# Optimization experiments

Measured on AMD Instinct MI355X. Metric: run time of the kernel, lower is better.

Reference implementation:

```python
import jax, jax.numpy as jnp
import numpy as np

B, N, H_IN, H_HID, N_HEAD = 32, 500, 64, 16, 8
N_VALID = 400  # valid (non-padded) nodes per graph; node 0 is the root
NEG_INF = -1e20


def setup_inputs() -> dict:
    key = jax.random.key(0)
    ks = jax.random.split(key, 10)
    x = jax.random.normal(ks[0], (B, N, H_IN), jnp.float32)
    # sparse-ish binary adjacency with self loops
    A = (jax.random.uniform(ks[1], (B, N, N)) < 0.05).astype(jnp.float32)
    A = jnp.maximum(A, jnp.eye(N, dtype=jnp.float32)[None])
    # mask_nonzero: first N_VALID nodes of every graph are valid
    mask_batch = jnp.repeat(jnp.arange(B, dtype=jnp.int32), N_VALID)
    mask_row = jnp.tile(jnp.arange(N_VALID, dtype=jnp.int32), B)
    s = 0.1
    w1 = jax.random.normal(ks[2], (N_HEAD, H_IN, H_HID), jnp.float32) * s
    a_src1 = jax.random.normal(ks[3], (N_HEAD, H_HID), jnp.float32) * s
    a_dst1 = jax.random.normal(ks[4], (N_HEAD, H_HID), jnp.float32) * s
    w2 = jax.random.normal(ks[5], (1, N_HEAD * H_HID, H_IN), jnp.float32) * s
    a_src2 = jax.random.normal(ks[6], (1, H_IN), jnp.float32) * s
    a_dst2 = jax.random.normal(ks[7], (1, H_IN), jnp.float32) * s
    attn_w = jax.random.normal(ks[8], (2 * H_IN,), jnp.float32) * s
    return {"x": x, "A": A, "mask_batch": mask_batch, "mask_row": mask_row,
            "w1": w1, "a_src1": a_src1, "a_dst1": a_dst1,
            "w2": w2, "a_src2": a_src2, "a_dst2": a_dst2, "attn_w": attn_w}


def gat_layer(h_in, A, w, a_src, a_dst):
    # h_in: [B,N,F_in]; w: [H,F_in,F_out]
    h = jnp.einsum('bnf,hfo->bhno', h_in, w)              # [B,H,N,F_out]
    e_src = jnp.einsum('bhno,ho->bhn', h, a_src)          # [B,H,N]
    e_dst = jnp.einsum('bhno,ho->bhn', h, a_dst)
    e = jax.nn.leaky_relu(e_src[..., :, None] + e_dst[..., None, :], 0.2)  # [B,H,N,N]
    e = jnp.where(A[:, None, :, :] > 0, e, NEG_INF)
    attn = jax.nn.softmax(e, axis=-1)
    return jnp.einsum('bhnm,bhmo->bhno', attn, h)         # [B,H,N,F_out]


def reference(x, A, mask_batch, mask_row, w1, a_src1, a_dst1, w2, a_src2, a_dst2, attn_w):
    b, n, _ = x.shape
    # BatchGAT encoder: layer 1 (multi-head, concat + ELU), layer 2 (1 head -> h_in)
    h1 = gat_layer(x, A, w1, a_src1, a_dst1)                       # [B,H,N,h_hid]
    h1 = jax.nn.elu(h1).transpose(0, 2, 1, 3).reshape(b, n, -1)    # [B,N,H*h_hid]
    xc = gat_layer(h1, A, w2, a_src2, a_dst2)[:, 0]                # [B,N,h_in]
    # zero out padded nodes (so their Post_Attn scores are exactly 0)
    valid = jnp.zeros((b, n), x.dtype).at[mask_batch, mask_row].set(1.0)
    xc = xc * valid[:, :, None]
    # Post_Attn: scatter root features to each valid node position
    root = jnp.zeros_like(xc).at[mask_batch, mask_row, :].set(xc[mask_batch, 0, :])
    x_plus = jnp.concatenate([xc, root], axis=-1)                  # [B,N,2*h_in]
    score = x_plus @ attn_w                                        # [B,N]
    score = jnp.where(score == 0, NEG_INF, score)[:, :, None]      # masked_fill
    attn = jax.nn.softmax(score, axis=1)                           # softmax over nodes
    pooled = jnp.einsum('bnf,bn->bf', xc, attn[:, :, 0])           # [B,h_in]
    return pooled, attn
```

## Files before the change

### kernel.cpp

```cpp
#include <hip/hip_runtime.h>

#define NB 32
#define NN 500
#define HIN 64
#define HHID 16
#define NHEAD 8
#define NVALID 400
#define MAXK 128
#define NEG_INF -1e20f

__global__ __launch_bounds__(256) void k_pre(const float* __restrict__ A,
                                             int* __restrict__ nbr, int* __restrict__ cnt,
                                             const float* __restrict__ x, const float* __restrict__ w1,
                                             const float* __restrict__ as1, const float* __restrict__ ad1,
                                             float* __restrict__ h1p, float* __restrict__ e1s,
                                             float* __restrict__ e1d)
{
    int bid = blockIdx.x;
    if (bid < 4000) {
        int row = bid * 4 + (threadIdx.x >> 6);
        int lane = threadIdx.x & 63;
        const float4* arow4 = (const float4*)(A + (size_t)row * NN);
        int* np = nbr + (size_t)row * MAXK;
        int c = 0;
#pragma unroll
        for (int it = 0; it < 2; ++it) {
            int idx = it * 64 + lane;
            float4 av;
            if (idx < 125) av = arow4[idx];
            else { av.x = av.y = av.z = av.w = 0.f; }
            bool v0 = av.x > 0.f, v1 = av.y > 0.f, v2 = av.z > 0.f, v3 = av.w > 0.f;
            unsigned long long b0 = __ballot(v0), b1 = __ballot(v1);
            unsigned long long b2 = __ballot(v2), b3 = __ballot(v3);
            unsigned long long below = (1ull << lane) - 1ull;
            int p = c + __popcll(b0 & below) + __popcll(b1 & below)
                      + __popcll(b2 & below) + __popcll(b3 & below);
            int col = idx * 4;
            if (v0 && p < MAXK) np[p] = col;     p += (int)v0;
            if (v1 && p < MAXK) np[p] = col + 1; p += (int)v1;
            if (v2 && p < MAXK) np[p] = col + 2; p += (int)v2;
            if (v3 && p < MAXK) np[p] = col + 3; p += (int)v3;
            c += (int)(__popcll(b0) + __popcll(b1) + __popcll(b2) + __popcll(b3));
        }
        if (lane == 0) cnt[row] = c < MAXK ? c : MAXK;
        return;
    }
    int pb = bid - 4000;
    int b = pb >> 5, chunk = pb & 31;
    int t = threadIdx.x, slot = t >> 7, lane = t & 127;
    int h = lane >> 4, o = lane & 15;
    float wreg[64];
#pragma unroll
    for (int f = 0; f < 64; ++f) wreg[f] = w1[h * 1024 + f * 16 + o];
    float as_r = as1[h * 16 + o], ad_r = ad1[h * 16 + o];
    __shared__ __align__(16) float xs[2][64];
    for (int i = 0; i < 8; ++i) {
        int n = chunk * 16 + i * 2 + slot;
        bool valid = n < NN;
        if (valid && lane < 64) xs[slot][lane] = x[(size_t)(b * NN + n) * HIN + lane];
        __syncthreads();
        if (valid) {
            float acc = 0.f;
#pragma unroll
            for (int f4 = 0; f4 < 16; ++f4) {
                float4 xv = *(const float4*)&xs[slot][f4 * 4];
                acc += xv.x * wreg[f4 * 4] + xv.y * wreg[f4 * 4 + 1]
                     + xv.z * wreg[f4 * 4 + 2] + xv.w * wreg[f4 * 4 + 3];
            }
            h1p[(size_t)(b * NN + n) * 128 + lane] = acc;
            float vs = acc * as_r, vd = acc * ad_r;
#pragma unroll
            for (int m = 1; m < 16; m <<= 1) { vs += __shfl_xor(vs, m); vd += __shfl_xor(vd, m); }
            if (o == 0) {
                e1s[(size_t)(b * NN + n) * 8 + h] = vs;
                e1d[(size_t)(b * NN + n) * 8 + h] = vd;
            }
        }
        __syncthreads();
    }
}

__global__ __launch_bounds__(128) void k_agg1(const int* __restrict__ nbr, const int* __restrict__ cnt,
                                              const float* __restrict__ h1p, const float* __restrict__ e1s,
                                              const float* __restrict__ e1d, float* __restrict__ h1cat)
{
    int row = blockIdx.x;
    int b = row / NN, n = row - b * NN;
    (void)n;
    int t = threadIdx.x;
    int h = t >> 4, o = t & 15;
    __shared__ int nb_s[MAXK];
    __shared__ float p_s[NHEAD][MAXK];
    int K = cnt[row];
    for (int k = t; k < K; k += 128) nb_s[k] = nbr[(size_t)row * MAXK + k];
    __syncthreads();
    float es = e1s[(size_t)row * 8 + h];
    float r[8];
    float mx = -1e30f;
#pragma unroll
    for (int j = 0; j < 8; ++j) {
        int k = o + j * 16;
        if (k < K) {
            float e = es + e1d[(size_t)(b * NN + nb_s[k]) * 8 + h];
            e = e > 0.f ? e : 0.2f * e;
            r[j] = e;
            mx = fmaxf(mx, e);
        }
    }
#pragma unroll
    for (int m = 1; m < 16; m <<= 1) mx = fmaxf(mx, __shfl_xor(mx, m));
    float sum = 0.f;
#pragma unroll
    for (int j = 0; j < 8; ++j) {
        int k = o + j * 16;
        if (k < K) { float v = __expf(r[j] - mx); r[j] = v; sum += v; }
    }
#pragma unroll
    for (int m = 1; m < 16; m <<= 1) sum += __shfl_xor(sum, m);
    float inv = 1.f / sum;
#pragma unroll
    for (int j = 0; j < 8; ++j) {
        int k = o + j * 16;
        if (k < K) p_s[h][k] = r[j] * inv;
    }
    __syncthreads();
    float acc = 0.f;
    const float* hp = h1p + (size_t)b * NN * 128 + t;
    for (int k = 0; k < K; ++k) acc += p_s[h][k] * hp[(size_t)nb_s[k] * 128];
    float outv = acc > 0.f ? acc : expm1f(acc);
    h1cat[(size_t)row * 128 + t] = outv;
}

__global__ __launch_bounds__(256) void k_proj2(const float* __restrict__ h1cat, const float* __restrict__ w2,
                                               const float* __restrict__ as2, const float* __restrict__ ad2,
                                               float* __restrict__ h2p, float* __restrict__ e2s,
                                               float* __restrict__ e2d)
{
    int b = blockIdx.y, chunk = blockIdx.x;
    int t = threadIdx.x, slot = t >> 7, lane = t & 127;
    int fh = lane >> 6, o = lane & 63;
    float wreg[64];
#pragma unroll
    for (int j = 0; j < 64; ++j) wreg[j] = w2[(fh * 64 + j) * 64 + o];
    float as_r = as2[o], ad_r = ad2[o];
    __shared__ __align__(16) float xs[2][128];
    __shared__ float part[2][128];
    for (int i = 0; i < 8; ++i) {
        int n = chunk * 16 + i * 2 + slot;
        bool valid = n < NN;
        if (valid) xs[slot][lane] = h1cat[(size_t)(b * NN + n) * 128 + lane];
        __syncthreads();
        float acc = 0.f;
        if (valid) {
#pragma unroll
            for (int j4 = 0; j4 < 16; ++j4) {
                float4 xv = *(const float4*)&xs[slot][fh * 64 + j4 * 4];
                acc += xv.x * wreg[j4 * 4] + xv.y * wreg[j4 * 4 + 1]
                     + xv.z * wreg[j4 * 4 + 2] + xv.w * wreg[j4 * 4 + 3];
            }
        }
        part[slot][lane] = acc;
        __syncthreads();
        if (valid && fh == 0) {
            float val = acc + part[slot][64 + o];
            h2p[(size_t)(b * NN + n) * 64 + o] = val;
            float vs = val * as_r, vd = val * ad_r;
#pragma unroll
            for (int m = 1; m < 64; m <<= 1) { vs += __shfl_xor(vs, m); vd += __shfl_xor(vd, m); }
            if (o == 0) { e2s[b * NN + n] = vs; e2d[b * NN + n] = vd; }
        }
        __syncthreads();
    }
}

__global__ __launch_bounds__(64) void k_agg2(const int* __restrict__ nbr, const int* __restrict__ cnt,
                                             const float* __restrict__ h2p, const float* __restrict__ e2s,
                                             const float* __restrict__ e2d, const float* __restrict__ aw,
                                             float* __restrict__ xc, float* __restrict__ sc,
                                             float* __restrict__ root_dot)
{
    int row = blockIdx.x;
    int b = row / NN, n = row - b * NN;
    int t = threadIdx.x;
    if (n >= NVALID) { xc[(size_t)row * 64 + t] = 0.f; return; }
    __shared__ int nb_s[MAXK];
    __shared__ float p_s[MAXK];
    int K = cnt[row];
    for (int k = t; k < K; k += 64) nb_s[k] = nbr[(size_t)row * MAXK + k];
    __syncthreads();
    float es = e2s[row];
    float r0 = -1e30f, r1 = -1e30f;
    if (t < K) {
        float e = es + e2d[b * NN + nb_s[t]];
        r0 = e > 0.f ? e : 0.2f * e;
    }
    if (t + 64 < K) {
        float e = es + e2d[b * NN + nb_s[t + 64]];
        r1 = e > 0.f ? e : 0.2f * e;
    }
    float mx = fmaxf(r0, r1);
#pragma unroll
    for (int m = 1; m < 64; m <<= 1) mx = fmaxf(mx, __shfl_xor(mx, m));
    float v0 = (t < K) ? __expf(r0 - mx) : 0.f;
    float v1 = (t + 64 < K) ? __expf(r1 - mx) : 0.f;
    float sum = v0 + v1;
#pragma unroll
    for (int m = 1; m < 64; m <<= 1) sum += __shfl_xor(sum, m);
    float inv = 1.f / sum;
    if (t < K) p_s[t] = v0 * inv;
    if (t + 64 < K) p_s[t + 64] = v1 * inv;
    __syncthreads();
    float acc = 0.f;
    for (int k = 0; k < K; ++k) acc += p_s[k] * h2p[(size_t)(b * NN + nb_s[k]) * 64 + t];
    xc[(size_t)row * 64 + t] = acc;
    float v = acc * aw[t];
#pragma unroll
    for (int m = 1; m < 64; m <<= 1) v += __shfl_xor(v, m);
    if (t == 0) sc[row] = v;
    if (n == 0) {
        float v2 = acc * aw[64 + t];
#pragma unroll
        for (int m = 1; m < 64; m <<= 1) v2 += __shfl_xor(v2, m);
        if (t == 0) root_dot[b] = v2;
    }
}

__global__ __launch_bounds__(1024) void k_pool(const float* __restrict__ xc, const float* __restrict__ sc,
                                               const float* __restrict__ root_dot, float* __restrict__ out)
{
    int b = blockIdx.x;
    int t = threadIdx.x, w = t >> 6, lane = t & 63;
    __shared__ float attn_s[NN];
    __shared__ float red[16];
    __shared__ float part[16][64];
    const float* xb = xc + (size_t)b * NN * 64;
    float rd = root_dot[b];
    float s = NEG_INF;
    if (t < NVALID) {
        s = sc[b * NN + t] + rd;
        if (s == 0.f) s = NEG_INF;
    }
    float mx = s;
#pragma unroll
    for (int m = 1; m < 64; m <<= 1) mx = fmaxf(mx, __shfl_xor(mx, m));
    if (lane == 0) red[w] = mx;
    __syncthreads();
    mx = red[0];
#pragma unroll
    for (int i = 1; i < 16; ++i) mx = fmaxf(mx, red[i]);
    float e = (t < NN) ? __expf(s - mx) : 0.f;
    float sum = e;
#pragma unroll
    for (int m = 1; m < 64; m <<= 1) sum += __shfl_xor(sum, m);
    __syncthreads();
    if (lane == 0) red[w] = sum;
    __syncthreads();
    sum = 0.f;
#pragma unroll
    for (int i = 0; i < 16; ++i) sum += red[i];
    float inv = 1.f / sum;
    if (t < NN) {
        float a = e * inv;
        out[NB * 64 + b * NN + t] = a;
        attn_s[t] = a;
    }
    __syncthreads();
    float acc = 0.f;
    for (int n = w; n < NN; n += 16) acc += attn_s[n] * xb[(size_t)n * 64 + lane];
    part[w][lane] = acc;
    __syncthreads();
    if (t < 64) {
        float v = 0.f;
#pragma unroll
        for (int i = 0; i < 16; ++i) v += part[i][t];
        out[b * 64 + t] = v;
    }
}

extern "C" void kernel_launch(void* const* d_in, const int* in_sizes, int n_in,
                              void* d_out, int out_size, void* d_ws, size_t ws_size,
                              hipStream_t stream) {
    const float* x   = (const float*)d_in[0];
    const float* A   = (const float*)d_in[1];
    const float* w1  = (const float*)d_in[4];
    const float* as1 = (const float*)d_in[5];
    const float* ad1 = (const float*)d_in[6];
    const float* w2  = (const float*)d_in[7];
    const float* as2 = (const float*)d_in[8];
    const float* ad2 = (const float*)d_in[9];
    const float* aw  = (const float*)d_in[10];
    float* out = (float*)d_out;

    char* ws = (char*)d_ws;
    int* nbr = (int*)ws;
    int* cnt = (int*)(ws + (size_t)16000 * 128 * 4);
    float* f = (float*)(ws + (size_t)16000 * 129 * 4);
    float* h1p   = f;  f += (size_t)NB * NN * 128;
    float* e1s   = f;  f += (size_t)NB * NN * NHEAD;
    float* e1d   = f;  f += (size_t)NB * NN * NHEAD;
    float* h1cat = f;  f += (size_t)NB * NN * 128;
    float* h2p   = f;  f += (size_t)NB * NN * 64;
    float* e2s   = f;  f += (size_t)NB * NN;
    float* e2d   = f;  f += (size_t)NB * NN;
    float* xc    = f;  f += (size_t)NB * NN * 64;
    float* sc    = f;  f += (size_t)NB * NN;
    float* rootd = f;  f += NB;

    hipLaunchKernelGGL(k_pre,   dim3(5024),   dim3(256), 0, stream, A, nbr, cnt, x, w1, as1, ad1, h1p, e1s, e1d);
    hipLaunchKernelGGL(k_agg1,  dim3(NB * NN), dim3(128), 0, stream, nbr, cnt, h1p, e1s, e1d, h1cat);
    hipLaunchKernelGGL(k_proj2, dim3(32, NB), dim3(256), 0, stream, h1cat, w2, as2, ad2, h2p, e2s, e2d);
    hipLaunchKernelGGL(k_agg2,  dim3(NB * NN), dim3(64), 0, stream, nbr, cnt, h2p, e2s, e2d, aw, xc, sc, rootd);
    hipLaunchKernelGGL(k_pool,  dim3(NB),     dim3(1024), 0, stream, xc, sc, rootd, out);
}
```

Measured before the change: 169.5 us.

## Fuse layer-2 projection into aggregation and pooling into last-block epilogue

Folds the layer-2 projection (h1cat @ w2 plus attention logits) into the layer-1 aggregation kernel, so the h1cat intermediate is no longer written to and read back from global memory. The final pooling kernel is merged into the layer-2 aggregation using a per-graph atomic counter, and the last block to finish each graph does the softmax and weighted sum. This takes five launches down to three. In exchange, every aggregation block now loads 64 weights per thread, and the pooling tail runs on a single 64-thread block per graph, which serialises the 500-node reduction.

```diff
diff --git a/kernel.cpp b/kernel.cpp
--- a/kernel.cpp
+++ b/kernel.cpp
@@ -14,9 +14,10 @@
                                              const float* __restrict__ x, const float* __restrict__ w1,
                                              const float* __restrict__ as1, const float* __restrict__ ad1,
                                              float* __restrict__ h1p, float* __restrict__ e1s,
-                                             float* __restrict__ e1d)
+                                             float* __restrict__ e1d, int* __restrict__ poolcnt)
 {
     int bid = blockIdx.x;
+    if (bid == 0 && threadIdx.x < NB) poolcnt[threadIdx.x] = 0;
     if (bid < 4000) {
         int row = bid * 4 + (threadIdx.x >> 6);
         int lane = threadIdx.x & 63;
@@ -80,17 +81,26 @@
     }
 }
 
-__global__ __launch_bounds__(128) void k_agg1(const int* __restrict__ nbr, const int* __restrict__ cnt,
-                                              const float* __restrict__ h1p, const float* __restrict__ e1s,
-                                              const float* __restrict__ e1d, float* __restrict__ h1cat)
+__global__ __launch_bounds__(128) void k_mid(const int* __restrict__ nbr, const int* __restrict__ cnt,
+                                             const float* __restrict__ h1p, const float* __restrict__ e1s,
+                                             const float* __restrict__ e1d, const float* __restrict__ w2,
+                                             const float* __restrict__ as2, const float* __restrict__ ad2,
+                                             float* __restrict__ h2p, float* __restrict__ e2s,
+                                             float* __restrict__ e2d)
 {
     int row = blockIdx.x;
-    int b = row / NN, n = row - b * NN;
-    (void)n;
+    int b = row / NN;
     int t = threadIdx.x;
     int h = t >> 4, o = t & 15;
+    int half = t >> 6, o2 = t & 63;
+    float wreg[64];
+    const float* wp = w2 + (size_t)(half * 64) * 64 + o2;
+#pragma unroll
+    for (int j = 0; j < 64; ++j) wreg[j] = wp[j * 64];
     __shared__ int nb_s[MAXK];
     __shared__ float p_s[NHEAD][MAXK];
+    __shared__ float hc[128];
+    __shared__ float part[128];
     int K = cnt[row];
     for (int k = t; k < K; k += 128) nb_s[k] = nbr[(size_t)row * MAXK + k];
     __syncthreads();
@@ -127,154 +137,134 @@
     float acc = 0.f;
     const float* hp = h1p + (size_t)b * NN * 128 + t;
     for (int k = 0; k < K; ++k) acc += p_s[h][k] * hp[(size_t)nb_s[k] * 128];
-    float outv = acc > 0.f ? acc : expm1f(acc);
-    h1cat[(size_t)row * 128 + t] = outv;
+    hc[t] = acc > 0.f ? acc : expm1f(acc);
+    __syncthreads();
+    float acc2 = 0.f;
+#pragma unroll
+    for (int j = 0; j < 64; ++j) acc2 += hc[half * 64 + j] * wreg[j];
+    part[t] = acc2;
+    __syncthreads();
+    if (half == 0) {
+        float val = acc2 + part[64 + o2];
+        h2p[(size_t)row * 64 + o2] = val;
+        float vs = val * as2[o2], vd = val * ad2[o2];
+#pragma unroll
+        for (int m = 1; m < 64; m <<= 1) { vs += __shfl_xor(vs, m); vd += __shfl_xor(vd, m); }
+        if (o2 == 0) { e2s[row] = vs; e2d[row] = vd; }
+    }
 }
 
-__global__ __launch_bounds__(256) void k_proj2(const float* __restrict__ h1cat, const float* __restrict__ w2,
-                                               const float* __restrict__ as2, const float* __restrict__ ad2,
-                                               float* __restrict__ h2p, float* __restrict__ e2s,
-                                               float* __restrict__ e2d)
-{
-    int b = blockIdx.y, chunk = blockIdx.x;
-    int t = threadIdx.x, slot = t >> 7, lane = t & 127;
-    int fh = lane >> 6, o = lane & 63;
-    float wreg[64];
-#pragma unroll
-    for (int j = 0; j < 64; ++j) wreg[j] = w2[(fh * 64 + j) * 64 + o];
-    float as_r = as2[o], ad_r = ad2[o];
-    __shared__ __align__(16) float xs[2][128];
-    __shared__ float part[2][128];
-    for (int i = 0; i < 8; ++i) {
-        int n = chunk * 16 + i * 2 + slot;
-        bool valid = n < NN;
-        if (valid) xs[slot][lane] = h1cat[(size_t)(b * NN + n) * 128 + lane];
-        __syncthreads();
-        float acc = 0.f;
-        if (valid) {
-#pragma unroll
-            for (int j4 = 0; j4 < 16; ++j4) {
-                float4 xv = *(const float4*)&xs[slot][fh * 64 + j4 * 4];
-                acc += xv.x * wreg[j4 * 4] + xv.y * wreg[j4 * 4 + 1]
-                     + xv.z * wreg[j4 * 4 + 2] + xv.w * wreg[j4 * 4 + 3];
-            }
-        }
-        part[slot][lane] = acc;
-        __syncthreads();
-        if (valid && fh == 0) {
-            float val = acc + part[slot][64 + o];
-            h2p[(size_t)(b * NN + n) * 64 + o] = val;
-            float vs = val * as_r, vd = val * ad_r;
-#pragma unroll
-            for (int m = 1; m < 64; m <<= 1) { vs += __shfl_xor(vs, m); vd += __shfl_xor(vd, m); }
-            if (o == 0) { e2s[b * NN + n] = vs; e2d[b * NN + n] = vd; }
-        }
-        __syncthreads();
-    }
-}
-
-__global__ __launch_bounds__(64) void k_agg2(const int* __restrict__ nbr, const int* __restrict__ cnt,
+__global__ __launch_bounds__(64) void k_last(const int* __restrict__ nbr, const int* __restrict__ cnt,
                                              const float* __restrict__ h2p, const float* __restrict__ e2s,
                                              const float* __restrict__ e2d, const float* __restrict__ aw,
                                              float* __restrict__ xc, float* __restrict__ sc,
-                                             float* __restrict__ root_dot)
+                                             float* __restrict__ root_dot, int* __restrict__ poolcnt,
+                                             float* __restrict__ out)
 {
     int row = blockIdx.x;
     int b = row / NN, n = row - b * NN;
     int t = threadIdx.x;
-    if (n >= NVALID) { xc[(size_t)row * 64 + t] = 0.f; return; }
     __shared__ int nb_s[MAXK];
     __shared__ float p_s[MAXK];
-    int K = cnt[row];
-    for (int k = t; k < K; k += 64) nb_s[k] = nbr[(size_t)row * MAXK + k];
-    __syncthreads();
-    float es = e2s[row];
-    float r0 = -1e30f, r1 = -1e30f;
-    if (t < K) {
-        float e = es + e2d[b * NN + nb_s[t]];
-        r0 = e > 0.f ? e : 0.2f * e;
-    }
-    if (t + 64 < K) {
-        float e = es + e2d[b * NN + nb_s[t + 64]];
-        r1 = e > 0.f ? e : 0.2f * e;
-    }
-    float mx = fmaxf(r0, r1);
-#pragma unroll
-    for (int m = 1; m < 64; m <<= 1) mx = fmaxf(mx, __shfl_xor(mx, m));
-    float v0 = (t < K) ? __expf(r0 - mx) : 0.f;
-    float v1 = (t + 64 < K) ? __expf(r1 - mx) : 0.f;
-    float sum = v0 + v1;
-#pragma unroll
-    for (int m = 1; m < 64; m <<= 1) sum += __shfl_xor(sum, m);
-    float inv = 1.f / sum;
-    if (t < K) p_s[t] = v0 * inv;
-    if (t + 64 < K) p_s[t + 64] = v1 * inv;
-    __syncthreads();
-    float acc = 0.f;
-    for (int k = 0; k < K; ++k) acc += p_s[k] * h2p[(size_t)(b * NN + nb_s[k]) * 64 + t];
-    xc[(size_t)row * 64 + t] = acc;
-    float v = acc * aw[t];
-#pragma unroll
-    for (int m = 1; m < 64; m <<= 1) v += __shfl_xor(v, m);
-    if (t == 0) sc[row] = v;
-    if (n == 0) {
-        float v2 = acc * aw[64 + t];
-#pragma unroll
-        for (int m = 1; m < 64; m <<= 1) v2 += __shfl_xor(v2, m);
-        if (t == 0) root_dot[b] = v2;
-    }
-}
-
-__global__ __launch_bounds__(1024) void k_pool(const float* __restrict__ xc, const float* __restrict__ sc,
-                                               const float* __restrict__ root_dot, float* __restrict__ out)
-{
-    int b = blockIdx.x;
-    int t = threadIdx.x, w = t >> 6, lane = t & 63;
     __shared__ float attn_s[NN];
-    __shared__ float red[16];
-    __shared__ float part[16][64];
+    __shared__ int isLast;
+    if (n >= NVALID) {
+        xc[(size_t)row * 64 + t] = 0.f;
+    } else {
+        int K = cnt[row];
+        for (int k = t; k < K; k += 64) nb_s[k] = nbr[(size_t)row * MAXK + k];
+        __syncthreads();
+        float es = e2s[row];
+        float r0 = -1e30f, r1 = -1e30f;
+        if (t < K) {
+            float e = es + e2d[b * NN + nb_s[t]];
+            r0 = e > 0.f ? e : 0.2f * e;
+        }
+        if (t + 64 < K) {
+            float e = es + e2d[b * NN + nb_s[t + 64]];
+            r1 = e > 0.f ? e : 0.2f * e;
+        }
+        float mx = fmaxf(r0, r1);
+#pragma unroll
+        for (int m = 1; m < 64; m <<= 1) mx = fmaxf(mx, __shfl_xor(mx, m));
+        float v0 = (t < K) ? __expf(r0 - mx) : 0.f;
+        float v1 = (t + 64 < K) ? __expf(r1 - mx) : 0.f;
+        float sum = v0 + v1;
+#pragma unroll
+        for (int m = 1; m < 64; m <<= 1) sum += __shfl_xor(sum, m);
+        float inv = 1.f / sum;
+        if (t < K) p_s[t] = v0 * inv;
+        if (t + 64 < K) p_s[t + 64] = v1 * inv;
+        __syncthreads();
+        float acc = 0.f;
+        for (int k = 0; k < K; ++k) acc += p_s[k] * h2p[(size_t)(b * NN + nb_s[k]) * 64 + t];
+        xc[(size_t)row * 64 + t] = acc;
+        float v = acc * aw[t];
+#pragma unroll
+        for (int m = 1; m < 64; m <<= 1) v += __shfl_xor(v, m);
+        if (t == 0) sc[row] = v;
+        if (n == 0) {
+            float v2 = acc * aw[64 + t];
+#pragma unroll
+            for (int m = 1; m < 64; m <<= 1) v2 += __shfl_xor(v2, m);
+            if (t == 0) root_dot[b] = v2;
+        }
+    }
+    __threadfence();
+    if (t == 0) {
+        int old = atomicAdd(&poolcnt[b], 1);
+        isLast = (old == NN - 1);
+    }
+    __syncthreads();
+    if (!isLast) return;
+    __threadfence();
+    const float* scb = sc + b * NN;
     const float* xb = xc + (size_t)b * NN * 64;
     float rd = root_dot[b];
-    float s = NEG_INF;
-    if (t < NVALID) {
-        s = sc[b * NN + t] + rd;
-        if (s == 0.f) s = NEG_INF;
-    }
-    float mx = s;
+    float sreg[8];
+    float mx = -1e30f;
+#pragma unroll
+    for (int j = 0; j < 8; ++j) {
+        int nn = j * 64 + t;
+        float s = NEG_INF;
+        if (nn < NVALID) {
+            s = scb[nn] + rd;
+            if (s == 0.f) s = NEG_INF;
+        }
+        sreg[j] = s;
+        mx = fmaxf(mx, s);
+    }
 #pragma unroll
     for (int m = 1; m < 64; m <<= 1) mx = fmaxf(mx, __shfl_xor(mx, m));
-    if (lane == 0) red[w] = mx;
-    __syncthreads();
-    mx = red[0];
-#pragma unroll
-    for (int i = 1; i < 16; ++i) mx = fmaxf(mx, red[i]);
-    float e = (t < NN) ? __expf(s - mx) : 0.f;
-    float sum = e;
-#pragma unroll
-    for (int m = 1; m < 64; m <<= 1) sum += __shfl_xor(sum, m);
-    __syncthreads();
-    if (lane == 0) red[w] = sum;
-    __syncthreads();
-    sum = 0.f;
-#pragma unroll
-    for (int i = 0; i < 16; ++i) sum += red[i];
+    float sum = 0.f;
+#pragma unroll
+    for (int j = 0; j < 8; ++j) {
+        int nn = j * 64 + t;
+        float e = (nn < NN) ? __expf(sreg[j] - mx) : 0.f;
+        sreg[j] = e;
+        float wsum = e;
+#pragma unroll
+        for (int m = 1; m < 64; m <<= 1) wsum += __shfl_xor(wsum, m);
+        sum += wsum;
+    }
     float inv = 1.f / sum;
-    if (t < NN) {
-        float a = e * inv;
-        out[NB * 64 + b * NN + t] = a;
-        attn_s[t] = a;
-    }
-    __syncthreads();
-    float acc = 0.f;
-    for (int n = w; n < NN; n += 16) acc += attn_s[n] * xb[(size_t)n * 64 + lane];
-    part[w][lane] = acc;
-    __syncthreads();
-    if (t < 64) {
-        float v = 0.f;
-#pragma unroll
-        for (int i = 0; i < 16; ++i) v += part[i][t];
-        out[b * 64 + t] = v;
-    }
+#pragma unroll
+    for (int j = 0; j < 8; ++j) {
+        int nn = j * 64 + t;
+        if (nn < NN) {
+            float a = sreg[j] * inv;
+            out[NB * 64 + b * NN + nn] = a;
+            attn_s[nn] = a;
+        }
+    }
+    __syncthreads();
+    float v = 0.f;
+    for (int w = 0; w < 16; ++w) {
+        float a = 0.f;
+        for (int nn = w; nn < NN; nn += 16) a += attn_s[nn] * xb[(size_t)nn * 64 + t];
+        v += a;
+    }
+    out[b * 64 + t] = v;
 }
 
 extern "C" void kernel_launch(void* const* d_in, const int* in_sizes, int n_in,
@@ -298,17 +288,15 @@
     float* h1p   = f;  f += (size_t)NB * NN * 128;
     float* e1s   = f;  f += (size_t)NB * NN * NHEAD;
     float* e1d   = f;  f += (size_t)NB * NN * NHEAD;
-    float* h1cat = f;  f += (size_t)NB * NN * 128;
     float* h2p   = f;  f += (size_t)NB * NN * 64;
     float* e2s   = f;  f += (size_t)NB * NN;
     float* e2d   = f;  f += (size_t)NB * NN;
     float* xc    = f;  f += (size_t)NB * NN * 64;
     float* sc    = f;  f += (size_t)NB * NN;
     float* rootd = f;  f += NB;
-
-    hipLaunchKernelGGL(k_pre,   dim3(5024),   dim3(256), 0, stream, A, nbr, cnt, x, w1, as1, ad1, h1p, e1s, e1d);
-    hipLaunchKernelGGL(k_agg1,  dim3(NB * NN), dim3(128), 0, stream, nbr, cnt, h1p, e1s, e1d, h1cat);
-    hipLaunchKernelGGL(k_proj2, dim3(32, NB), dim3(256), 0, stream, h1cat, w2, as2, ad2, h2p, e2s, e2d);
-    hipLaunchKernelGGL(k_agg2,  dim3(NB * NN), dim3(64), 0, stream, nbr, cnt, h2p, e2s, e2d, aw, xc, sc, rootd);
-    hipLaunchKernelGGL(k_pool,  dim3(NB),     dim3(1024), 0, stream, xc, sc, rootd, out);
+    int* poolcnt = (int*)f;
+
+    hipLaunchKernelGGL(k_pre,  dim3(5024),    dim3(256), 0, stream, A, nbr, cnt, x, w1, as1, ad1, h1p, e1s, e1d, poolcnt);
+    hipLaunchKernelGGL(k_mid,  dim3(NB * NN), dim3(128), 0, stream, nbr, cnt, h1p, e1s, e1d, w2, as2, ad2, h2p, e2s, e2d);
+    hipLaunchKernelGGL(k_last, dim3(NB * NN), dim3(64),  0, stream, nbr, cnt, h2p, e2s, e2d, aw, xc, sc, rootd, poolcnt, out);
 }
```

New measurement: 535.6 us. +216.0%, slower.

## Make both GAT aggregation kernels persistent, two rows per block, unrolled gathers

Applied to the files above, without the earlier changes.

Both neighbour-aggregation kernels now run a fixed grid of 2048 blocks that grid-stride over pairs of rows, with each half-block or wavefront owning one row. This replaces one small block per row. The gather of neighbour features is unrolled by four so several independent global loads are in flight at once. The second-layer kernel drops its block barriers and relies on wavefront-synchronous execution for the LDS neighbour list and probabilities. That saves sync cost but depends on implicit lockstep ordering of LDS accesses within a wave.

```diff
diff --git a/kernel.cpp b/kernel.cpp
--- a/kernel.cpp
+++ b/kernel.cpp
@@ -80,55 +80,67 @@
     }
 }
 
-__global__ __launch_bounds__(128) void k_agg1(const int* __restrict__ nbr, const int* __restrict__ cnt,
+__global__ __launch_bounds__(256) void k_agg1(const int* __restrict__ nbr, const int* __restrict__ cnt,
                                               const float* __restrict__ h1p, const float* __restrict__ e1s,
                                               const float* __restrict__ e1d, float* __restrict__ h1cat)
 {
-    int row = blockIdx.x;
-    int b = row / NN, n = row - b * NN;
-    (void)n;
-    int t = threadIdx.x;
+    int half = threadIdx.x >> 7, t = threadIdx.x & 127;
     int h = t >> 4, o = t & 15;
-    __shared__ int nb_s[MAXK];
-    __shared__ float p_s[NHEAD][MAXK];
-    int K = cnt[row];
-    for (int k = t; k < K; k += 128) nb_s[k] = nbr[(size_t)row * MAXK + k];
-    __syncthreads();
-    float es = e1s[(size_t)row * 8 + h];
-    float r[8];
-    float mx = -1e30f;
-#pragma unroll
-    for (int j = 0; j < 8; ++j) {
-        int k = o + j * 16;
-        if (k < K) {
-            float e = es + e1d[(size_t)(b * NN + nb_s[k]) * 8 + h];
-            e = e > 0.f ? e : 0.2f * e;
-            r[j] = e;
-            mx = fmaxf(mx, e);
-        }
-    }
-#pragma unroll
-    for (int m = 1; m < 16; m <<= 1) mx = fmaxf(mx, __shfl_xor(mx, m));
-    float sum = 0.f;
-#pragma unroll
-    for (int j = 0; j < 8; ++j) {
-        int k = o + j * 16;
-        if (k < K) { float v = __expf(r[j] - mx); r[j] = v; sum += v; }
-    }
-#pragma unroll
-    for (int m = 1; m < 16; m <<= 1) sum += __shfl_xor(sum, m);
-    float inv = 1.f / sum;
-#pragma unroll
-    for (int j = 0; j < 8; ++j) {
-        int k = o + j * 16;
-        if (k < K) p_s[h][k] = r[j] * inv;
-    }
-    __syncthreads();
-    float acc = 0.f;
-    const float* hp = h1p + (size_t)b * NN * 128 + t;
-    for (int k = 0; k < K; ++k) acc += p_s[h][k] * hp[(size_t)nb_s[k] * 128];
-    float outv = acc > 0.f ? acc : expm1f(acc);
-    h1cat[(size_t)row * 128 + t] = outv;
+    __shared__ int nb_s[2][MAXK];
+    __shared__ float p_s[2][NHEAD][MAXK + 4];
+    for (int pair = blockIdx.x; pair < NB * NN / 2; pair += gridDim.x) {
+        int row = pair * 2 + half;
+        int b = row / NN;
+        int K = cnt[row];
+        for (int k = t; k < K; k += 128) nb_s[half][k] = nbr[(size_t)row * MAXK + k];
+        __syncthreads();
+        float es = e1s[(size_t)row * 8 + h];
+        float r[8];
+        float mx = -1e30f;
+#pragma unroll
+        for (int j = 0; j < 8; ++j) {
+            int k = o + j * 16;
+            if (k < K) {
+                float e = es + e1d[(size_t)(b * NN + nb_s[half][k]) * 8 + h];
+                e = e > 0.f ? e : 0.2f * e;
+                r[j] = e;
+                mx = fmaxf(mx, e);
+            }
+        }
+#pragma unroll
+        for (int m = 1; m < 16; m <<= 1) mx = fmaxf(mx, __shfl_xor(mx, m));
+        float sum = 0.f;
+#pragma unroll
+        for (int j = 0; j < 8; ++j) {
+            int k = o + j * 16;
+            if (k < K) { float v = __expf(r[j] - mx); r[j] = v; sum += v; }
+        }
+#pragma unroll
+        for (int m = 1; m < 16; m <<= 1) sum += __shfl_xor(sum, m);
+        float inv = 1.f / sum;
+#pragma unroll
+        for (int j = 0; j < 8; ++j) {
+            int k = o + j * 16;
+            if (k < K) p_s[half][h][k] = r[j] * inv;
+        }
+        __syncthreads();
+        float acc = 0.f;
+        const float* hp = h1p + (size_t)b * NN * 128 + t;
+        int k = 0;
+        for (; k + 4 <= K; k += 4) {
+            float a0 = hp[(size_t)nb_s[half][k] * 128];
+            float a1 = hp[(size_t)nb_s[half][k + 1] * 128];
+            float a2 = hp[(size_t)nb_s[half][k + 2] * 128];
+            float a3 = hp[(size_t)nb_s[half][k + 3] * 128];
+            acc += p_s[half][h][k] * a0;
+            acc += p_s[half][h][k + 1] * a1;
+            acc += p_s[half][h][k + 2] * a2;
+            acc += p_s[half][h][k + 3] * a3;
+        }
+        for (; k < K; ++k) acc += p_s[half][h][k] * hp[(size_t)nb_s[half][k] * 128];
+        h1cat[(size_t)row * 128 + t] = acc > 0.f ? acc : expm1f(acc);
+        __syncthreads();
+    }
 }
 
 __global__ __launch_bounds__(256) void k_proj2(const float* __restrict__ h1cat, const float* __restrict__ w2,
@@ -173,55 +185,71 @@
     }
 }
 
-__global__ __launch_bounds__(64) void k_agg2(const int* __restrict__ nbr, const int* __restrict__ cnt,
-                                             const float* __restrict__ h2p, const float* __restrict__ e2s,
-                                             const float* __restrict__ e2d, const float* __restrict__ aw,
-                                             float* __restrict__ xc, float* __restrict__ sc,
-                                             float* __restrict__ root_dot)
-{
-    int row = blockIdx.x;
-    int b = row / NN, n = row - b * NN;
-    int t = threadIdx.x;
-    if (n >= NVALID) { xc[(size_t)row * 64 + t] = 0.f; return; }
-    __shared__ int nb_s[MAXK];
-    __shared__ float p_s[MAXK];
-    int K = cnt[row];
-    for (int k = t; k < K; k += 64) nb_s[k] = nbr[(size_t)row * MAXK + k];
-    __syncthreads();
-    float es = e2s[row];
-    float r0 = -1e30f, r1 = -1e30f;
-    if (t < K) {
-        float e = es + e2d[b * NN + nb_s[t]];
-        r0 = e > 0.f ? e : 0.2f * e;
-    }
-    if (t + 64 < K) {
-        float e = es + e2d[b * NN + nb_s[t + 64]];
-        r1 = e > 0.f ? e : 0.2f * e;
-    }
-    float mx = fmaxf(r0, r1);
-#pragma unroll
-    for (int m = 1; m < 64; m <<= 1) mx = fmaxf(mx, __shfl_xor(mx, m));
-    float v0 = (t < K) ? __expf(r0 - mx) : 0.f;
-    float v1 = (t + 64 < K) ? __expf(r1 - mx) : 0.f;
-    float sum = v0 + v1;
-#pragma unroll
-    for (int m = 1; m < 64; m <<= 1) sum += __shfl_xor(sum, m);
-    float inv = 1.f / sum;
-    if (t < K) p_s[t] = v0 * inv;
-    if (t + 64 < K) p_s[t + 64] = v1 * inv;
-    __syncthreads();
-    float acc = 0.f;
-    for (int k = 0; k < K; ++k) acc += p_s[k] * h2p[(size_t)(b * NN + nb_s[k]) * 64 + t];
-    xc[(size_t)row * 64 + t] = acc;
-    float v = acc * aw[t];
-#pragma unroll
-    for (int m = 1; m < 64; m <<= 1) v += __shfl_xor(v, m);
-    if (t == 0) sc[row] = v;
-    if (n == 0) {
-        float v2 = acc * aw[64 + t];
-#pragma unroll
-        for (int m = 1; m < 64; m <<= 1) v2 += __shfl_xor(v2, m);
-        if (t == 0) root_dot[b] = v2;
+__global__ __launch_bounds__(128) void k_agg2(const int* __restrict__ nbr, const int* __restrict__ cnt,
+                                              const float* __restrict__ h2p, const float* __restrict__ e2s,
+                                              const float* __restrict__ e2d, const float* __restrict__ aw,
+                                              float* __restrict__ xc, float* __restrict__ sc,
+                                              float* __restrict__ root_dot)
+{
+    int w = threadIdx.x >> 6, t = threadIdx.x & 63;
+    __shared__ int nb_s[2][MAXK];
+    __shared__ float p_s[2][MAXK];
+    float aw0 = aw[t], aw1 = aw[64 + t];
+    for (int pair = blockIdx.x; pair < NB * NN / 2; pair += gridDim.x) {
+        int row = pair * 2 + w;
+        int b = row / NN, n = row - b * NN;
+        if (n >= NVALID) {
+            xc[(size_t)row * 64 + t] = 0.f;
+            continue;
+        }
+        int K = cnt[row];
+        for (int k = t; k < K; k += 64) nb_s[w][k] = nbr[(size_t)row * MAXK + k];
+        float es = e2s[row];
+        float r0 = -1e30f, r1 = -1e30f;
+        if (t < K) {
+            float e = es + e2d[b * NN + nb_s[w][t]];
+            r0 = e > 0.f ? e : 0.2f * e;
+        }
+        if (t + 64 < K) {
+            float e = es + e2d[b * NN + nb_s[w][t + 64]];
+            r1 = e > 0.f ? e : 0.2f * e;
+        }
+        float mx = fmaxf(r0, r1);
+#pragma unroll
+        for (int m = 1; m < 64; m <<= 1) mx = fmaxf(mx, __shfl_xor(mx, m));
+        float v0 = (t < K) ? __expf(r0 - mx) : 0.f;
+        float v1 = (t + 64 < K) ? __expf(r1 - mx) : 0.f;
+        float sum = v0 + v1;
+#pragma unroll
+        for (int m = 1; m < 64; m <<= 1) sum += __shfl_xor(sum, m);
+        float inv = 1.f / sum;
+        if (t < K) p_s[w][t] = v0 * inv;
+        if (t + 64 < K) p_s[w][t + 64] = v1 * inv;
+        float acc = 0.f;
+        const float* h2b = h2p + (size_t)b * NN * 64 + t;
+        int k = 0;
+        for (; k + 4 <= K; k += 4) {
+            float a0 = h2b[(size_t)nb_s[w][k] * 64];
+            float a1 = h2b[(size_t)nb_s[w][k + 1] * 64];
+            float a2 = h2b[(size_t)nb_s[w][k + 2] * 64];
+            float a3 = h2b[(size_t)nb_s[w][k + 3] * 64];
+            acc += p_s[w][k] * a0;
+            acc += p_s[w][k + 1] * a1;
+            acc += p_s[w][k + 2] * a2;
+            acc += p_s[w][k + 3] * a3;
+        }
+        for (; k < K; ++k) acc += p_s[w][k] * h2b[(size_t)nb_s[w][k] * 64];
+        xc[(size_t)row * 64 + t] = acc;
+        float v = acc * aw0;
+#pragma unroll
+        for (int m = 1; m < 64; m <<= 1) v += __shfl_xor(v, m);
+        if (t == 0) sc[row] = v;
+        if (n == 0) {
+            float v2 = acc * aw1;
+#pragma unroll
+            for (int m = 1; m < 64; m <<= 1) v2 += __shfl_xor(v2, m);
+            if (t == 0) root_dot[b] = v2;
+        }
     }
 }
 
@@ -306,9 +334,9 @@
     float* sc    = f;  f += (size_t)NB * NN;
     float* rootd = f;  f += NB;
 
-    hipLaunchKernelGGL(k_pre,   dim3(5024),   dim3(256), 0, stream, A, nbr, cnt, x, w1, as1, ad1, h1p, e1s, e1d);
-    hipLaunchKernelGGL(k_agg1,  dim3(NB * NN), dim3(128), 0, stream, nbr, cnt, h1p, e1s, e1d, h1cat);
+    hipLaunchKernelGGL(k_pre,   dim3(5024), dim3(256), 0, stream, A, nbr, cnt, x, w1, as1, ad1, h1p, e1s, e1d);
+    hipLaunchKernelGGL(k_agg1,  dim3(2048), dim3(256), 0, stream, nbr, cnt, h1p, e1s, e1d, h1cat);
     hipLaunchKernelGGL(k_proj2, dim3(32, NB), dim3(256), 0, stream, h1cat, w2, as2, ad2, h2p, e2s, e2d);
-    hipLaunchKernelGGL(k_agg2,  dim3(NB * NN), dim3(64), 0, stream, nbr, cnt, h2p, e2s, e2d, aw, xc, sc, rootd);
-    hipLaunchKernelGGL(k_pool,  dim3(NB),     dim3(1024), 0, stream, xc, sc, rootd, out);
-}
+    hipLaunchKernelGGL(k_agg2,  dim3(2048), dim3(128), 0, stream, nbr, cnt, h2p, e2s, e2d, aw, xc, sc, rootd);
+    hipLaunchKernelGGL(k_pool,  dim3(NB),   dim3(1024), 0, stream, xc, sc, rootd, out);
+}
```

After: 186.3 us. 9.9% more time.
